# Kernel optimization log

Measured on AMD Instinct MI355X. Metric: run time of the kernel, lower is better.

## Reference

```python
import jax, jax.numpy as jnp
import numpy as np

B, S, D = 4, 2048, 2048
H = 16
Q_LORA = 1536
KV_LORA = 512
D_NOPE = 128
D_ROPE = 64
D_V = 128
MLP = 8192
EPS = 1e-6
THETA = 10000.0


def rmsnorm(x, scale, eps=EPS):
    var = jnp.mean(jnp.square(x.astype(jnp.float32)), axis=-1, keepdims=True)
    return (x * jax.lax.rsqrt(var + eps)).astype(x.dtype) * scale


def rope(x, positions):
    # x: [B, S, H, d], positions: [B, S]
    d = x.shape[-1]
    inv_freq = 1.0 / (THETA ** (jnp.arange(0, d, 2, dtype=jnp.float32) / d))
    ang = positions.astype(jnp.float32)[..., None] * inv_freq  # [B,S,d/2]
    cos = jnp.cos(ang)[:, :, None, :]
    sin = jnp.sin(ang)[:, :, None, :]
    x1, x2 = jnp.split(x, 2, axis=-1)
    return jnp.concatenate([x1 * cos - x2 * sin, x2 * cos + x1 * sin], axis=-1)


def setup_inputs() -> dict:
    key = jax.random.key(0)
    ks = jax.random.split(key, 16)
    sd = lambda fan: 1.0 / np.sqrt(fan)
    inp = {
        'inputs': jax.random.normal(ks[0], (B, S, D), jnp.float32),
        'decoder_segment_ids': jnp.ones((B, S), jnp.int32),
        'decoder_positions': jnp.broadcast_to(jnp.arange(S, dtype=jnp.int32), (B, S)),
        'pre_ln_scale': jnp.ones((D,), jnp.float32),
        'post_ln_scale': jnp.ones((D,), jnp.float32),
        'q_ln_scale': jnp.ones((Q_LORA,), jnp.float32),
        'kv_ln_scale': jnp.ones((KV_LORA,), jnp.float32),
        'wq_a': jax.random.normal(ks[1], (D, Q_LORA), jnp.float32) * sd(D),
        'wq_b': jax.random.normal(ks[2], (Q_LORA, H, D_NOPE + D_ROPE), jnp.float32) * sd(Q_LORA),
        'wkv_a': jax.random.normal(ks[3], (D, KV_LORA + D_ROPE), jnp.float32) * sd(D),
        'wkv_b': jax.random.normal(ks[4], (KV_LORA, H, D_NOPE + D_V), jnp.float32) * sd(KV_LORA),
        'wo_attn': jax.random.normal(ks[5], (H, D_V, D), jnp.float32) * sd(H * D_V),
        'wi_0': jax.random.normal(ks[6], (D, MLP), jnp.float32) * sd(D),
        'wi_1': jax.random.normal(ks[7], (D, MLP), jnp.float32) * sd(D),
        'wo_mlp': jax.random.normal(ks[8], (MLP, D), jnp.float32) * sd(MLP),
    }
    return inp


def reference(inputs, decoder_segment_ids, decoder_positions, pre_ln_scale, post_ln_scale,
              q_ln_scale, kv_ln_scale, wq_a, wq_b, wkv_a, wkv_b, wo_attn, wi_0, wi_1, wo_mlp):
    # ---- pre-norm ----
    lnx = rmsnorm(inputs, pre_ln_scale)

    # ---- MLA attention ----
    # low-rank query: down-proj, norm, up-proj
    q_c = rmsnorm(lnx @ wq_a, q_ln_scale)                       # [B,S,Q_LORA]
    q = jnp.einsum('bsr,rhd->bshd', q_c, wq_b)                  # [B,S,H,nope+rope]
    q_nope, q_rope = q[..., :D_NOPE], q[..., D_NOPE:]

    # compressed kv + decoupled rope key
    kv = lnx @ wkv_a                                            # [B,S,KV_LORA+rope]
    c_kv = rmsnorm(kv[..., :KV_LORA], kv_ln_scale)
    k_rope = kv[..., KV_LORA:][:, :, None, :]                   # [B,S,1,rope]
    kvu = jnp.einsum('bsr,rhd->bshd', c_kv, wkv_b)              # [B,S,H,nope+v]
    k_nope, v = kvu[..., :D_NOPE], kvu[..., D_NOPE:]

    q_rope = rope(q_rope, decoder_positions)
    k_rope = rope(k_rope, decoder_positions)
    k_rope = jnp.broadcast_to(k_rope, (B, S, H, D_ROPE))

    qf = jnp.concatenate([q_nope, q_rope], axis=-1)             # [B,S,H,192]
    kf = jnp.concatenate([k_nope, k_rope], axis=-1)

    scale = 1.0 / np.sqrt(D_NOPE + D_ROPE)
    scores = jnp.einsum('bqhd,bkhd->bhqk', qf, kf) * scale      # [B,H,S,S]

    pos = decoder_positions
    seg = decoder_segment_ids
    mask = (pos[:, :, None] >= pos[:, None, :]) & (seg[:, :, None] == seg[:, None, :])
    scores = jnp.where(mask[:, None, :, :], scores, -1e9)
    probs = jax.nn.softmax(scores, axis=-1)

    attn = jnp.einsum('bhqk,bkhd->bqhd', probs, v)              # [B,S,H,D_V]
    attn_out = jnp.einsum('bqhd,hdm->bqm', attn, wo_attn)       # [B,S,D]

    # ---- residual + post-norm ----
    intermediate = inputs + attn_out
    hidden = rmsnorm(intermediate, post_ln_scale)

    # ---- gated MLP (silu * linear) ----
    mlp = (jax.nn.silu(hidden @ wi_0) * (hidden @ wi_1)) @ wo_mlp

    return mlp + intermediate
```

## Files before the change

kernel.cpp:

```cpp
#include <hip/hip_runtime.h>
#include <stdint.h>

typedef unsigned short u16;
typedef __bf16 bf16x8 __attribute__((ext_vector_type(8)));
typedef float f32x4 __attribute__((ext_vector_type(4)));

#define B_ 4
#define S_ 2048
#define H_ 16
#define TOK (B_*S_)
#define MFMA_B16 __builtin_amdgcn_mfma_f32_16x16x32_bf16
#define LGKM0 asm volatile("s_waitcnt lgkmcnt(0)" ::: "memory")
#define VMC(n) asm volatile("s_waitcnt vmcnt(" #n ")" ::: "memory")

__device__ __forceinline__ u16 f32_bf16(float f) {
    union { float f; unsigned int u; } x; x.f = f;
    return (u16)((x.u + 0x7fffu + ((x.u >> 16) & 1u)) >> 16);
}
__device__ __forceinline__ float bf2f(u16 v) {
    union { unsigned int u; float f; } x; x.u = ((unsigned int)v) << 16; return x.f;
}
__device__ __forceinline__ void gld_lds16(const u16* g, u16* lds) {
    __builtin_amdgcn_global_load_lds(
        (const __attribute__((address_space(1))) unsigned int*)g,
        (__attribute__((address_space(3))) unsigned int*)lds, 16, 0, 0);
}

__global__ void fill_sentinel(float* o, int n) {
    int i = blockIdx.x * 256 + threadIdx.x;
    if (i < n) o[i] = 12345.0f;
}

__global__ __launch_bounds__(256) void transpose_f32_bf16(const float* __restrict__ in, u16* __restrict__ out,
                                                          int K, int N, int Npad) {
    __shared__ float t[32][33];
    int nb = blockIdx.x * 32, kb = blockIdx.y * 32;
    int c = threadIdx.x & 31, r = threadIdx.x >> 5;
#pragma unroll
    for (int i = 0; i < 4; ++i) {
        int kk = kb + r + i * 8, nn = nb + c;
        t[r + i * 8][c] = (kk < K && nn < N) ? in[(size_t)kk * N + nn] : 0.f;
    }
    __syncthreads();
#pragma unroll
    for (int i = 0; i < 4; ++i) {
        int no = nb + r + i * 8, ko = kb + c;
        if (no < Npad && ko < K) out[(size_t)no * K + ko] = f32_bf16(t[c][r + i * 8]);
    }
}

__global__ __launch_bounds__(256) void rmsnorm_f32(const float* __restrict__ in, const float* __restrict__ sc,
                                                   u16* __restrict__ out, int N) {
    int row = blockIdx.x;
    const float* x = in + (size_t)row * N;
    float ss = 0.f;
    for (int c = threadIdx.x * 4; c < N; c += 1024) {
        float4 v = *(const float4*)(x + c);
        ss += v.x * v.x + v.y * v.y + v.z * v.z + v.w * v.w;
    }
#pragma unroll
    for (int off = 32; off; off >>= 1) ss += __shfl_down(ss, off);
    __shared__ float red[4];
    if ((threadIdx.x & 63) == 0) red[threadIdx.x >> 6] = ss;
    __syncthreads();
    float rs = rsqrtf((red[0] + red[1] + red[2] + red[3]) / (float)N + 1e-6f);
    for (int c = threadIdx.x * 4; c < N; c += 1024) {
        float4 v = *(const float4*)(x + c);
        float4 s4 = *(const float4*)(sc + c);
        ushort4 ov;
        ov.x = f32_bf16(v.x * rs * s4.x);
        ov.y = f32_bf16(v.y * rs * s4.y);
        ov.z = f32_bf16(v.z * rs * s4.z);
        ov.w = f32_bf16(v.w * rs * s4.w);
        *(ushort4*)&out[(size_t)row * N + c] = ov;
    }
}

__global__ __launch_bounds__(256) void rmsnorm_bf16(const u16* __restrict__ in, const float* __restrict__ sc,
                                                    u16* __restrict__ out, int N) {
    int row = blockIdx.x;
    const u16* x = in + (size_t)row * N;
    float ss = 0.f;
    for (int c = threadIdx.x * 8; c < N; c += 2048) {
        ushort4 v0 = *(const ushort4*)(x + c);
        ushort4 v1 = *(const ushort4*)(x + c + 4);
        float f0 = bf2f(v0.x), f1 = bf2f(v0.y), f2 = bf2f(v0.z), f3 = bf2f(v0.w);
        float f4 = bf2f(v1.x), f5 = bf2f(v1.y), f6 = bf2f(v1.z), f7 = bf2f(v1.w);
        ss += f0*f0 + f1*f1 + f2*f2 + f3*f3 + f4*f4 + f5*f5 + f6*f6 + f7*f7;
    }
#pragma unroll
    for (int off = 32; off; off >>= 1) ss += __shfl_down(ss, off);
    __shared__ float red[4];
    if ((threadIdx.x & 63) == 0) red[threadIdx.x >> 6] = ss;
    __syncthreads();
    float rs = rsqrtf((red[0] + red[1] + red[2] + red[3]) / (float)N + 1e-6f);
    for (int c = threadIdx.x * 8; c < N; c += 2048) {
        ushort4 v0 = *(const ushort4*)(x + c);
        ushort4 v1 = *(const ushort4*)(x + c + 4);
        ushort4 o0, o1;
        o0.x = f32_bf16(bf2f(v0.x) * rs * sc[c + 0]);
        o0.y = f32_bf16(bf2f(v0.y) * rs * sc[c + 1]);
        o0.z = f32_bf16(bf2f(v0.z) * rs * sc[c + 2]);
        o0.w = f32_bf16(bf2f(v0.w) * rs * sc[c + 3]);
        o1.x = f32_bf16(bf2f(v1.x) * rs * sc[c + 4]);
        o1.y = f32_bf16(bf2f(v1.y) * rs * sc[c + 5]);
        o1.z = f32_bf16(bf2f(v1.z) * rs * sc[c + 6]);
        o1.w = f32_bf16(bf2f(v1.w) * rs * sc[c + 7]);
        *(ushort4*)&out[(size_t)row * N + c] = o0;
        *(ushort4*)&out[(size_t)row * N + c + 4] = o1;
    }
}

__global__ __launch_bounds__(128) void kv_post(const u16* __restrict__ kv, const float* __restrict__ scale,
                                               const int* __restrict__ pos, u16* __restrict__ ckv,
                                               u16* __restrict__ kr) {
    int row = blockIdx.x;
    const u16* x = kv + (size_t)row * 640;
    int c = threadIdx.x * 4;
    ushort4 v = *(const ushort4*)(x + c);
    float f0 = bf2f(v.x), f1 = bf2f(v.y), f2 = bf2f(v.z), f3 = bf2f(v.w);
    float ss = f0*f0 + f1*f1 + f2*f2 + f3*f3;
#pragma unroll
    for (int off = 32; off; off >>= 1) ss += __shfl_down(ss, off);
    __shared__ float red[2];
    if ((threadIdx.x & 63) == 0) red[threadIdx.x >> 6] = ss;
    __syncthreads();
    float rs = rsqrtf((red[0] + red[1]) * (1.f / 512.f) + 1e-6f);
    float4 s4 = *(const float4*)(scale + c);
    ushort4 ov;
    ov.x = f32_bf16(f0 * rs * s4.x);
    ov.y = f32_bf16(f1 * rs * s4.y);
    ov.z = f32_bf16(f2 * rs * s4.z);
    ov.w = f32_bf16(f3 * rs * s4.w);
    *(ushort4*)&ckv[(size_t)row * 512 + c] = ov;
    if (threadIdx.x < 32) {
        int i = threadIdx.x;
        float x1 = bf2f(x[512 + i]), x2 = bf2f(x[544 + i]);
        float inv = expf(-(float)(2 * i) * (1.f / 64.f) * 9.2103403719761836f);
        float ang = (float)pos[row] * inv;
        float sn, cs; sincosf(ang, &sn, &cs);
        kr[(size_t)row * 64 + i]      = f32_bf16(x1 * cs - x2 * sn);
        kr[(size_t)row * 64 + 32 + i] = f32_bf16(x2 * cs + x1 * sn);
    }
}

__global__ __launch_bounds__(64) void q_rope_inplace(u16* __restrict__ q, const int* __restrict__ pos) {
    int token = blockIdx.x, h = blockIdx.y;
    u16* p = q + ((size_t)token * 16 + h) * 192;
    int t = threadIdx.x, i = t & 31;
    float x1 = bf2f(p[128 + i]), x2 = bf2f(p[160 + i]);
    float inv = expf(-(float)(2 * i) * (1.f / 64.f) * 9.2103403719761836f);
    float ang = (float)pos[token] * inv;
    float sn, cs; sincosf(ang, &sn, &cs);
    float val = (t < 32) ? (x1 * cs - x2 * sn) : (x2 * cs + x1 * sn);
    p[128 + t] = f32_bf16(val);
}

__global__ __launch_bounds__(320) void kv_build(const u16* __restrict__ kvu, const u16* __restrict__ kr,
                                                u16* __restrict__ kf, u16* __restrict__ vf, int tok0) {
    int local = blockIdx.x, h = blockIdx.y;
    int token = tok0 + local;
    int b = token >> 11, s = token & 2047;
    int bh = b * 16 + h;
    int tile = s >> 6, ki = s & 63;
    const u16* u = kvu + ((size_t)local * 16 + h) * 256;
    int t = threadIdx.x;
    if (t < 192) {
        u16 val = (t < 128) ? u[t] : kr[(size_t)token * 64 + (t - 128)];
        int byte = (ki * 384 + t * 2) ^ ((ki & 7) << 4);
        kf[(size_t)bh * (S_ * 192) + (size_t)tile * 12288 + (byte >> 1)] = val;
    } else {
        int dv = t - 192;
        u16 val = u[128 + dv];
        int byte = (dv * 128 + ki * 2) ^ ((dv & 7) << 4);
        vf[(size_t)bh * (S_ * 128) + (size_t)tile * 8192 + (byte >> 1)] = val;
    }
}

__global__ __launch_bounds__(256) void gemm128(const u16* __restrict__ A, const u16* __restrict__ Bt,
                                               u16* __restrict__ C, int M, int N, int K) {
    __shared__ u16 As[128 * 32];
    __shared__ u16 Bs[128 * 32];
    const int l = threadIdx.x & 63, w = threadIdx.x >> 6;
    const int wr = w >> 1, wc = w & 1;
    const int m0 = blockIdx.y * 128, n0 = blockIdx.x * 128;
    const int lm = l & 15, lg = l >> 4;
    const int srow = l >> 2, sk = (l & 3) * 8;
    f32x4 acc[4][4] = {};
    for (int k0 = 0; k0 < K; k0 += 32) {
#pragma unroll
        for (int i = 0; i < 2; ++i) {
            int c = w * 2 + i;
            gld_lds16(A  + (size_t)(m0 + c * 16 + srow) * K + k0 + sk, &As[c * 512]);
            gld_lds16(Bt + (size_t)(n0 + c * 16 + srow) * K + k0 + sk, &Bs[c * 512]);
        }
        __syncthreads();
        bf16x8 a[4], b[4];
#pragma unroll
        for (int m = 0; m < 4; ++m) a[m] = *(const bf16x8*)&As[(wr * 64 + m * 16 + lm) * 32 + lg * 8];
#pragma unroll
        for (int n = 0; n < 4; ++n) b[n] = *(const bf16x8*)&Bs[(wc * 64 + n * 16 + lm) * 32 + lg * 8];
#pragma unroll
        for (int m = 0; m < 4; ++m)
#pragma unroll
            for (int n = 0; n < 4; ++n)
                acc[m][n] = MFMA_B16(a[m], b[n], acc[m][n], 0, 0, 0);
        __syncthreads();
    }
#pragma unroll
    for (int m = 0; m < 4; ++m)
#pragma unroll
        for (int j = 0; j < 4; ++j) {
            int row = m0 + wr * 64 + m * 16 + lg * 4 + j;
            size_t base = (size_t)row * N + n0 + wc * 64;
#pragma unroll
            for (int n = 0; n < 4; ++n)
                C[base + n * 16 + lm] = f32_bf16(acc[m][n][j]);
        }
}

template<int EPI>
__global__ __launch_bounds__(512, 1) void gemm256(const u16* __restrict__ A, const u16* __restrict__ Bt,
                                                  void* __restrict__ Cv, const void* __restrict__ Rv,
                                                  int M, int N, int K) {
    __shared__ u16 lds[65536];
    char* ldsb = (char*)lds;
    const int tid = threadIdx.x;
    const int l = tid & 63, w = tid >> 6;
    const int wr = w >> 2, wcn = w & 3;
    const int lm = l & 15, lg = l >> 4;

    const int gx = gridDim.x;
    const int nwg = gx * gridDim.y;
    const int lin = blockIdx.y * gx + blockIdx.x;
    const int swz = (lin & 7) * (nwg >> 3) + (lin >> 3);
    const int m0 = (swz / gx) * 256, n0 = (swz % gx) * 256;

    int sr[2], sc[2];
#pragma unroll
    for (int ld = 0; ld < 2; ++ld) {
        int P = tid * 16 + ld * 8192;
        sr[ld] = P >> 7;
        sc[ld] = (P & 127) ^ ((sr[ld] & 7) << 4);
    }
    const u16* Ab = A + (size_t)m0 * K;
    const u16* Bb = Bt + (size_t)n0 * K;

    f32x4 acc[8][4] = {};

    auto stage = [&](const u16* gp, int mb, int h, int t) {
#pragma unroll
        for (int ld = 0; ld < 2; ++ld)
            gld_lds16(gp + (size_t)(h * 128 + sr[ld]) * K + t * 64 + (sc[ld] >> 1),
                      (u16*)(ldsb + (t & 1) * 65536 + mb + h * 16384 + tid * 16 + ld * 8192));
    };
    auto readA = [&](int buf, int fm, int ks) -> bf16x8 {
        int m = wr * 128 + fm * 16 + lm;
        int r = m & 127;
        int byte = (ks * 64 + lg * 16) ^ ((r & 7) << 4);
        return *(const bf16x8*)(ldsb + buf * 65536 + (m >> 7) * 16384 + r * 128 + byte);
    };
    auto readB = [&](int buf, int fn, int ks) -> bf16x8 {
        int n = wcn * 64 + fn * 16 + lm;
        int r = n & 127;
        int byte = (ks * 64 + lg * 16) ^ ((r & 7) << 4);
        return *(const bf16x8*)(ldsb + buf * 65536 + 32768 + (n >> 7) * 16384 + r * 128 + byte);
    };

    const int nt = K >> 6;
    stage(Ab, 0, 0, 0); stage(Ab, 0, 1, 0);
    stage(Bb, 32768, 0, 0); stage(Bb, 32768, 1, 0);
    VMC(0);
    __builtin_amdgcn_s_barrier();

#pragma unroll 1
    for (int t = 0; t < nt; ++t) {
        const int buf = t & 1;
        const bool nx = (t + 1 < nt);
        bf16x8 a0, a1, a2, a3, a4, a5, a6, a7;
        bf16x8 b0 = readB(buf, 0, 0), b1 = readB(buf, 0, 1), b2 = readB(buf, 1, 0), b3 = readB(buf, 1, 1);
        a0 = readA(buf, 0, 0); a1 = readA(buf, 0, 1); a2 = readA(buf, 1, 0); a3 = readA(buf, 1, 1);
        a4 = readA(buf, 2, 0); a5 = readA(buf, 2, 1); a6 = readA(buf, 3, 0); a7 = readA(buf, 3, 1);
        if (nx) { stage(Ab, 0, 0, t + 1); stage(Ab, 0, 1, t + 1); }
        __builtin_amdgcn_s_barrier();
        LGKM0;
        __builtin_amdgcn_sched_barrier(0);
        __builtin_amdgcn_s_setprio(1);
        acc[0][0] = MFMA_B16(a0, b0, acc[0][0], 0, 0, 0);
        acc[0][0] = MFMA_B16(a1, b1, acc[0][0], 0, 0, 0);
        acc[0][1] = MFMA_B16(a0, b2, acc[0][1], 0, 0, 0);
        acc[0][1] = MFMA_B16(a1, b3, acc[0][1], 0, 0, 0);
        acc[1][0] = MFMA_B16(a2, b0, acc[1][0], 0, 0, 0);
        acc[1][0] = MFMA_B16(a3, b1, acc[1][0], 0, 0, 0);
        acc[1][1] = MFMA_B16(a2, b2, acc[1][1], 0, 0, 0);
        acc[1][1] = MFMA_B16(a3, b3, acc[1][1], 0, 0, 0);
        acc[2][0] = MFMA_B16(a4, b0, acc[2][0], 0, 0, 0);
        acc[2][0] = MFMA_B16(a5, b1, acc[2][0], 0, 0, 0);
        acc[2][1] = MFMA_B16(a4, b2, acc[2][1], 0, 0, 0);
        acc[2][1] = MFMA_B16(a5, b3, acc[2][1], 0, 0, 0);
        acc[3][0] = MFMA_B16(a6, b0, acc[3][0], 0, 0, 0);
        acc[3][0] = MFMA_B16(a7, b1, acc[3][0], 0, 0, 0);
        acc[3][1] = MFMA_B16(a6, b2, acc[3][1], 0, 0, 0);
        acc[3][1] = MFMA_B16(a7, b3, acc[3][1], 0, 0, 0);
        __builtin_amdgcn_s_setprio(0);
        __builtin_amdgcn_s_barrier();
        bf16x8 c0 = readB(buf, 2, 0), c1 = readB(buf, 2, 1), c2 = readB(buf, 3, 0), c3 = readB(buf, 3, 1);
        if (nx) { stage(Bb, 32768, 0, t + 1); stage(Bb, 32768, 1, t + 1); }
        __builtin_amdgcn_s_barrier();
        LGKM0;
        __builtin_amdgcn_sched_barrier(0);
        __builtin_amdgcn_s_setprio(1);
        acc[0][2] = MFMA_B16(a0, c0, acc[0][2], 0, 0, 0);
        acc[0][2] = MFMA_B16(a1, c1, acc[0][2], 0, 0, 0);
        acc[0][3] = MFMA_B16(a0, c2, acc[0][3], 0, 0, 0);
        acc[0][3] = MFMA_B16(a1, c3, acc[0][3], 0, 0, 0);
        acc[1][2] = MFMA_B16(a2, c0, acc[1][2], 0, 0, 0);
        acc[1][2] = MFMA_B16(a3, c1, acc[1][2], 0, 0, 0);
        acc[1][3] = MFMA_B16(a2, c2, acc[1][3], 0, 0, 0);
        acc[1][3] = MFMA_B16(a3, c3, acc[1][3], 0, 0, 0);
        acc[2][2] = MFMA_B16(a4, c0, acc[2][2], 0, 0, 0);
        acc[2][2] = MFMA_B16(a5, c1, acc[2][2], 0, 0, 0);
        acc[2][3] = MFMA_B16(a4, c2, acc[2][3], 0, 0, 0);
        acc[2][3] = MFMA_B16(a5, c3, acc[2][3], 0, 0, 0);
        acc[3][2] = MFMA_B16(a6, c0, acc[3][2], 0, 0, 0);
        acc[3][2] = MFMA_B16(a7, c1, acc[3][2], 0, 0, 0);
        acc[3][3] = MFMA_B16(a6, c2, acc[3][3], 0, 0, 0);
        acc[3][3] = MFMA_B16(a7, c3, acc[3][3], 0, 0, 0);
        __builtin_amdgcn_s_setprio(0);
        __builtin_amdgcn_s_barrier();
        a0 = readA(buf, 4, 0); a1 = readA(buf, 4, 1); a2 = readA(buf, 5, 0); a3 = readA(buf, 5, 1);
        a4 = readA(buf, 6, 0); a5 = readA(buf, 6, 1); a6 = readA(buf, 7, 0); a7 = readA(buf, 7, 1);
        __builtin_amdgcn_s_barrier();
        LGKM0;
        __builtin_amdgcn_sched_barrier(0);
        __builtin_amdgcn_s_setprio(1);
        acc[4][2] = MFMA_B16(a0, c0, acc[4][2], 0, 0, 0);
        acc[4][2] = MFMA_B16(a1, c1, acc[4][2], 0, 0, 0);
        acc[4][3] = MFMA_B16(a0, c2, acc[4][3], 0, 0, 0);
        acc[4][3] = MFMA_B16(a1, c3, acc[4][3], 0, 0, 0);
        acc[5][2] = MFMA_B16(a2, c0, acc[5][2], 0, 0, 0);
        acc[5][2] = MFMA_B16(a3, c1, acc[5][2], 0, 0, 0);
        acc[5][3] = MFMA_B16(a2, c2, acc[5][3], 0, 0, 0);
        acc[5][3] = MFMA_B16(a3, c3, acc[5][3], 0, 0, 0);
        acc[6][2] = MFMA_B16(a4, c0, acc[6][2], 0, 0, 0);
        acc[6][2] = MFMA_B16(a5, c1, acc[6][2], 0, 0, 0);
        acc[6][3] = MFMA_B16(a4, c2, acc[6][3], 0, 0, 0);
        acc[6][3] = MFMA_B16(a5, c3, acc[6][3], 0, 0, 0);
        acc[7][2] = MFMA_B16(a6, c0, acc[7][2], 0, 0, 0);
        acc[7][2] = MFMA_B16(a7, c1, acc[7][2], 0, 0, 0);
        acc[7][3] = MFMA_B16(a6, c2, acc[7][3], 0, 0, 0);
        acc[7][3] = MFMA_B16(a7, c3, acc[7][3], 0, 0, 0);
        __builtin_amdgcn_s_setprio(0);
        __builtin_amdgcn_s_barrier();
        VMC(0);
        __builtin_amdgcn_s_barrier();
        __builtin_amdgcn_s_setprio(1);
        acc[4][0] = MFMA_B16(a0, b0, acc[4][0], 0, 0, 0);
        acc[4][0] = MFMA_B16(a1, b1, acc[4][0], 0, 0, 0);
        acc[4][1] = MFMA_B16(a0, b2, acc[4][1], 0, 0, 0);
        acc[4][1] = MFMA_B16(a1, b3, acc[4][1], 0, 0, 0);
        acc[5][0] = MFMA_B16(a2, b0, acc[5][0], 0, 0, 0);
        acc[5][0] = MFMA_B16(a3, b1, acc[5][0], 0, 0, 0);
        acc[5][1] = MFMA_B16(a2, b2, acc[5][1], 0, 0, 0);
        acc[5][1] = MFMA_B16(a3, b3, acc[5][1], 0, 0, 0);
        acc[6][0] = MFMA_B16(a4, b0, acc[6][0], 0, 0, 0);
        acc[6][0] = MFMA_B16(a5, b1, acc[6][0], 0, 0, 0);
        acc[6][1] = MFMA_B16(a4, b2, acc[6][1], 0, 0, 0);
        acc[6][1] = MFMA_B16(a5, b3, acc[6][1], 0, 0, 0);
        acc[7][0] = MFMA_B16(a6, b0, acc[7][0], 0, 0, 0);
        acc[7][0] = MFMA_B16(a7, b1, acc[7][0], 0, 0, 0);
        acc[7][1] = MFMA_B16(a6, b2, acc[7][1], 0, 0, 0);
        acc[7][1] = MFMA_B16(a7, b3, acc[7][1], 0, 0, 0);
        __builtin_amdgcn_s_setprio(0);
        __builtin_amdgcn_s_barrier();
    }
#pragma unroll
    for (int fm = 0; fm < 8; ++fm)
#pragma unroll
        for (int j = 0; j < 4; ++j) {
            int row = m0 + wr * 128 + fm * 16 + lg * 4 + j;
            size_t base = (size_t)row * N + n0 + wcn * 64;
#pragma unroll
            for (int fn = 0; fn < 4; ++fn) {
                size_t idx = base + fn * 16 + lm;
                float v = acc[fm][fn][j];
                if (EPI == 0) {
                    ((u16*)Cv)[idx] = f32_bf16(v);
                } else if (EPI == 1) {
                    ((float*)Cv)[idx] = v + ((const float*)Rv)[idx];
                } else {
                    float x0 = bf2f(((const u16*)Rv)[idx]);
                    float sl = x0 / (1.f + expf(-x0));
                    ((u16*)Cv)[idx] = f32_bf16(sl * v);
                }
            }
        }
}

__global__ __launch_bounds__(256, 3) void attn_fwd(const u16* __restrict__ qf, const u16* __restrict__ kfs,
                                                   const u16* __restrict__ vfs, u16* __restrict__ attn) {
    __shared__ u16 Ks[64 * 192];
    __shared__ u16 Vs[128 * 64];
    __shared__ u16 Ps[4][1024];
    const int lin = blockIdx.y * gridDim.x + blockIdx.x;
    const int xcd = lin & 7, j = lin >> 3;
    const int bh = xcd * 8 + (j >> 4);
    const int px = j & 15;
    const int b = bh >> 4, h = bh & 15;
    const int l = threadIdx.x & 63, w = threadIdx.x >> 6;
    const int lm = l & 15, g = l >> 4;
    const u16* kb0 = kfs + (size_t)bh * (S_ * 192);
    const u16* vb0 = vfs + (size_t)bh * (S_ * 128);
    const float scale = 0.07216878364870322f;

    auto stageK = [&](int kt2) {
        const u16* kc = kb0 + (size_t)kt2 * 12288;
#pragma unroll
        for (int i = 0; i < 6; ++i) {
            int c = w + i * 4;
            gld_lds16(kc + c * 512 + l * 8, &Ks[c * 512]);
        }
    };
    auto stageV = [&](int kt2) {
        const u16* vc = vb0 + (size_t)kt2 * 8192;
#pragma unroll
        for (int i = 0; i < 4; ++i) {
            int c = w + i * 4;
            gld_lds16(vc + c * 512 + l * 8, &Vs[c * 512]);
        }
    };

    stageK(0);

    for (int pass = 0; pass < 2; ++pass) {
        const int qb = pass ? (31 - px) : px;
        const int qrow = qb * 64 + w * 16 + lm;
        const u16* qp = qf + (((size_t)(b * S_ + qrow)) * 16 + h) * 192 + g * 8;
        bf16x8 qr[6];
#pragma unroll
        for (int c = 0; c < 6; ++c) qr[c] = *(const bf16x8*)(qp + c * 32);
        f32x4 o[8] = {};
        float mrow[4] = {-1e30f, -1e30f, -1e30f, -1e30f};
        float lrow[4] = {0.f, 0.f, 0.f, 0.f};
        for (int kt = 0; kt <= qb; ++kt) {
            __syncthreads();
            stageV(kt);
            f32x4 sc[4] = {};
#pragma unroll
            for (int nf = 0; nf < 4; ++nf) {
                int key = nf * 16 + lm;
                int kswz = (key & 7) << 4;
#pragma unroll
                for (int c = 0; c < 6; ++c) {
                    int byte = (key * 384 + (c * 32 + g * 8) * 2) ^ kswz;
                    bf16x8 kv = *(const bf16x8*)((const char*)Ks + byte);
                    sc[nf] = MFMA_B16(qr[c], kv, sc[nf], 0, 0, 0);
                }
            }
            LGKM0;
            __builtin_amdgcn_s_barrier();
            if (kt < qb) stageK(kt + 1);
#pragma unroll
            for (int jj = 0; jj < 4; ++jj) {
                const int q_g = qb * 64 + w * 16 + g * 4 + jj;
                float mx = -1e30f;
#pragma unroll
                for (int nf = 0; nf < 4; ++nf) {
                    int key_g = kt * 64 + nf * 16 + lm;
                    float v = sc[nf][jj] * scale;
                    v = (key_g > q_g) ? -1e30f : v;
                    sc[nf][jj] = v;
                    mx = fmaxf(mx, v);
                }
                mx = fmaxf(mx, __shfl_xor(mx, 1));
                mx = fmaxf(mx, __shfl_xor(mx, 2));
                mx = fmaxf(mx, __shfl_xor(mx, 4));
                mx = fmaxf(mx, __shfl_xor(mx, 8));
                float newm = fmaxf(mrow[jj], mx);
                float fac = __expf(mrow[jj] - newm);
                mrow[jj] = newm;
                float rs = 0.f;
                u16 pb[4];
#pragma unroll
                for (int nf = 0; nf < 4; ++nf) {
                    float pv = __expf(sc[nf][jj] - newm);
                    rs += pv;
                    pb[nf] = f32_bf16(pv);
                }
                rs += __shfl_xor(rs, 1);
                rs += __shfl_xor(rs, 2);
                rs += __shfl_xor(rs, 4);
                rs += __shfl_xor(rs, 8);
                lrow[jj] = lrow[jj] * fac + rs;
#pragma unroll
                for (int n = 0; n < 8; ++n) o[n][jj] *= fac;
                int row = g * 4 + jj;
                int rswz = (row & 7) << 4;
#pragma unroll
                for (int nf = 0; nf < 4; ++nf) {
                    int byte = (row * 128 + (nf * 16 + lm) * 2) ^ rswz;
                    *(u16*)((char*)&Ps[w][0] + byte) = pb[nf];
                }
            }
            if (kt < qb) { VMC(6); } else { VMC(0); }
            __builtin_amdgcn_s_barrier();
            __builtin_amdgcn_sched_barrier(0);
#pragma unroll
            for (int kc2 = 0; kc2 < 2; ++kc2) {
                int pbyte = (lm * 128 + (kc2 * 32 + g * 8) * 2) ^ ((lm & 7) << 4);
                bf16x8 pa = *(const bf16x8*)((const char*)&Ps[w][0] + pbyte);
#pragma unroll
                for (int n = 0; n < 8; ++n) {
                    int dv = n * 16 + lm;
                    int vbyte = (dv * 128 + (kc2 * 32 + g * 8) * 2) ^ ((dv & 7) << 4);
                    bf16x8 vv = *(const bf16x8*)((const char*)Vs + vbyte);
                    o[n] = MFMA_B16(pa, vv, o[n], 0, 0, 0);
                }
            }
        }
#pragma unroll
        for (int jj = 0; jj < 4; ++jj) {
            float inv = 1.f / lrow[jj];
            int s = qb * 64 + w * 16 + g * 4 + jj;
            size_t base = ((size_t)(b * S_ + s)) * (H_ * 128) + h * 128;
#pragma unroll
            for (int n = 0; n < 8; ++n)
                attn[base + n * 16 + lm] = f32_bf16(o[n][jj] * inv);
        }
        if (pass == 0) stageK(0);
    }
}

extern "C" void kernel_launch(void* const* d_in, const int* in_sizes, int n_in,
                              void* d_out, int out_size, void* d_ws, size_t ws_size,
                              hipStream_t stream) {
    (void)in_sizes; (void)n_in;
    const float* inputs = (const float*)d_in[0];
    const int*   pos    = (const int*)d_in[2];
    const float* pre_s  = (const float*)d_in[3];
    const float* post_s = (const float*)d_in[4];
    const float* q_s    = (const float*)d_in[5];
    const float* kv_s   = (const float*)d_in[6];
    const float* wq_a   = (const float*)d_in[7];
    const float* wq_b   = (const float*)d_in[8];
    const float* wkv_a  = (const float*)d_in[9];
    const float* wkv_b  = (const float*)d_in[10];
    const float* wo_at  = (const float*)d_in[11];
    const float* wi0    = (const float*)d_in[12];
    const float* wi1    = (const float*)d_in[13];
    const float* wom    = (const float*)d_in[14];
    float* out = (float*)d_out;

    char* p = (char*)d_ws;
    auto alloc = [&](size_t n) { char* r = p; p += (n + 255) & ~(size_t)255; return r; };
    char* R1   = alloc((size_t)134217728);
    u16* vf    = (u16*)alloc((size_t)33554432);
    u16* aslot = (u16*)alloc((size_t)33554432);
    u16* wslot = (u16*)alloc((size_t)33554432);
    u16* ckv   = (u16*)alloc((size_t)8388608);
    u16* krope = (u16*)alloc((size_t)1048576);
    if ((size_t)(p - (char*)d_ws) > ws_size) {
        fill_sentinel<<<(out_size + 255) / 256, 256, 0, stream>>>(out, out_size);
        return;
    }
    u16* kf    = (u16*)R1;
    u16* q_c   = (u16*)R1;
    u16* kvtmp = (u16*)(R1 + 25165824);
    u16* q     = (u16*)(R1 + 50331648);
    u16* lnx   = (u16*)(R1 + 100663296);
    u16* kvu   = (u16*)(R1 + 100663296);
    u16* X     = (u16*)R1;

    rmsnorm_f32<<<TOK, 256, 0, stream>>>(inputs, pre_s, lnx, 2048);
    transpose_f32_bf16<<<dim3(48, 64), 256, 0, stream>>>(wq_a, wslot, 2048, 1536, 1536);
    gemm256<0><<<dim3(6, 32), 512, 0, stream>>>(lnx, wslot, q_c, nullptr, TOK, 1536, 2048);
    rmsnorm_bf16<<<TOK, 256, 0, stream>>>(q_c, q_s, q_c, 1536);
    transpose_f32_bf16<<<dim3(20, 64), 256, 0, stream>>>(wkv_a, wslot, 2048, 576, 640);
    gemm128<<<dim3(5, 64), 256, 0, stream>>>(lnx, wslot, kvtmp, TOK, 640, 2048);
    kv_post<<<TOK, 128, 0, stream>>>(kvtmp, kv_s, pos, ckv, krope);
    transpose_f32_bf16<<<dim3(96, 48), 256, 0, stream>>>(wq_b, wslot, 1536, 3072, 3072);
    gemm256<0><<<dim3(12, 32), 512, 0, stream>>>(q_c, wslot, q, nullptr, TOK, 3072, 1536);
    q_rope_inplace<<<dim3(TOK, 16), 64, 0, stream>>>(q, pos);
    transpose_f32_bf16<<<dim3(128, 16), 256, 0, stream>>>(wkv_b, wslot, 512, 4096, 4096);
    for (int ch = 0; ch < 2; ++ch) {
        int t0 = ch * 4096;
        gemm256<0><<<dim3(16, 16), 512, 0, stream>>>(ckv + (size_t)t0 * 512, wslot, kvu, nullptr, 4096, 4096, 512);
        kv_build<<<dim3(4096, 16), 320, 0, stream>>>(kvu, krope, kf, vf, t0);
    }
    attn_fwd<<<dim3(16, 64), 256, 0, stream>>>(q, kf, vf, aslot);
    transpose_f32_bf16<<<dim3(64, 64), 256, 0, stream>>>(wo_at, wslot, 2048, 2048, 2048);
    gemm256<1><<<dim3(8, 32), 512, 0, stream>>>(aslot, wslot, out, inputs, TOK, 2048, 2048);
    rmsnorm_f32<<<TOK, 256, 0, stream>>>(out, post_s, aslot, 2048);
    transpose_f32_bf16<<<dim3(256, 64), 256, 0, stream>>>(wi0, wslot, 2048, 8192, 8192);
    gemm256<0><<<dim3(32, 32), 512, 0, stream>>>(aslot, wslot, X, nullptr, TOK, 8192, 2048);
    transpose_f32_bf16<<<dim3(256, 64), 256, 0, stream>>>(wi1, wslot, 2048, 8192, 8192);
    gemm256<2><<<dim3(32, 32), 512, 0, stream>>>(aslot, wslot, X, X, TOK, 8192, 2048);
    transpose_f32_bf16<<<dim3(64, 256), 256, 0, stream>>>(wom, wslot, 8192, 2048, 2048);
    gemm256<1><<<dim3(8, 32), 512, 0, stream>>>(X, wslot, out, out, TOK, 2048, 8192);
}
```

Baseline: 1.666 ms.

## Restage GEMM LDS tiles into four quarter units with finer-grained vmcnt waits

The 256x256 GEMM's shared-memory staging is split into four 16KB units, each matched to the sub-tile a particular MFMA phase consumes. Each unit's next-tile prefetch is issued in a different phase, and partial vmcnt waits let compute start before all loads have landed, instead of one full wait per iteration. The swizzled workgroup-to-tile mapping is removed in favour of plain blockIdx mapping, which may change L2 reuse across workgroups. The new ordering assumes in-order vmcnt completion per unit, so the counts must exactly match the issue order.

```diff
diff --git a/kernel.cpp b/kernel.cpp
--- a/kernel.cpp
+++ b/kernel.cpp
@@ -12,6 +12,7 @@
 #define MFMA_B16 __builtin_amdgcn_mfma_f32_16x16x32_bf16
 #define LGKM0 asm volatile("s_waitcnt lgkmcnt(0)" ::: "memory")
 #define VMC(n) asm volatile("s_waitcnt vmcnt(" #n ")" ::: "memory")
+#define SB0 __builtin_amdgcn_sched_barrier(0)
 
 __device__ __forceinline__ u16 f32_bf16(float f) {
     union { float f; unsigned int u; } x; x.f = f;
@@ -229,48 +230,46 @@
     const int l = tid & 63, w = tid >> 6;
     const int wr = w >> 2, wcn = w & 3;
     const int lm = l & 15, lg = l >> 4;
-
-    const int gx = gridDim.x;
-    const int nwg = gx * gridDim.y;
-    const int lin = blockIdx.y * gx + blockIdx.x;
-    const int swz = (lin & 7) * (nwg >> 3) + (lin >> 3);
-    const int m0 = (swz / gx) * 256, n0 = (swz % gx) * 256;
-
-    int sr[2], sc[2];
+    const int m0 = blockIdx.y * 256, n0 = blockIdx.x * 256;
+
+    int sr[2], scb[2];
 #pragma unroll
     for (int ld = 0; ld < 2; ++ld) {
         int P = tid * 16 + ld * 8192;
         sr[ld] = P >> 7;
-        sc[ld] = (P & 127) ^ ((sr[ld] & 7) << 4);
+        scb[ld] = (P & 127) ^ ((sr[ld] & 7) << 4);
     }
     const u16* Ab = A + (size_t)m0 * K;
     const u16* Bb = Bt + (size_t)n0 * K;
 
     f32x4 acc[8][4] = {};
 
-    auto stage = [&](const u16* gp, int mb, int h, int t) {
-#pragma unroll
-        for (int ld = 0; ld < 2; ++ld)
-            gld_lds16(gp + (size_t)(h * 128 + sr[ld]) * K + t * 64 + (sc[ld] >> 1),
-                      (u16*)(ldsb + (t & 1) * 65536 + mb + h * 16384 + tid * 16 + ld * 8192));
+    auto stageU = [&](int unit, int tt) {
+#pragma unroll
+        for (int ld = 0; ld < 2; ++ld) {
+            int r = sr[ld];
+            const u16* src;
+            if (unit == 0)      src = Ab + (size_t)((r >> 6) * 128 + (r & 63)) * K + tt * 64 + (scb[ld] >> 1);
+            else if (unit == 1) src = Ab + (size_t)((r >> 6) * 128 + 64 + (r & 63)) * K + tt * 64 + (scb[ld] >> 1);
+            else if (unit == 2) src = Bb + (size_t)((r >> 5) * 64 + (r & 31)) * K + tt * 64 + (scb[ld] >> 1);
+            else                src = Bb + (size_t)((r >> 5) * 64 + 32 + (r & 31)) * K + tt * 64 + (scb[ld] >> 1);
+            gld_lds16(src, (u16*)(ldsb + (tt & 1) * 65536 + unit * 16384 + tid * 16 + ld * 8192));
+        }
     };
     auto readA = [&](int buf, int fm, int ks) -> bf16x8 {
-        int m = wr * 128 + fm * 16 + lm;
-        int r = m & 127;
-        int byte = (ks * 64 + lg * 16) ^ ((r & 7) << 4);
-        return *(const bf16x8*)(ldsb + buf * 65536 + (m >> 7) * 16384 + r * 128 + byte);
+        int lr = wr * 64 + (fm & 3) * 16 + lm;
+        int byte = lr * 128 + ((ks * 64 + lg * 16) ^ ((lr & 7) << 4));
+        return *(const bf16x8*)(ldsb + buf * 65536 + (fm >> 2) * 16384 + byte);
     };
     auto readB = [&](int buf, int fn, int ks) -> bf16x8 {
-        int n = wcn * 64 + fn * 16 + lm;
-        int r = n & 127;
-        int byte = (ks * 64 + lg * 16) ^ ((r & 7) << 4);
-        return *(const bf16x8*)(ldsb + buf * 65536 + 32768 + (n >> 7) * 16384 + r * 128 + byte);
+        int lr = wcn * 32 + (fn & 1) * 16 + lm;
+        int byte = lr * 128 + ((ks * 64 + lg * 16) ^ ((lr & 7) << 4));
+        return *(const bf16x8*)(ldsb + buf * 65536 + (2 + (fn >> 1)) * 16384 + byte);
     };
 
     const int nt = K >> 6;
-    stage(Ab, 0, 0, 0); stage(Ab, 0, 1, 0);
-    stage(Bb, 32768, 0, 0); stage(Bb, 32768, 1, 0);
-    VMC(0);
+    stageU(0, 0); stageU(2, 0); stageU(3, 0); stageU(1, 0);
+    VMC(2);
     __builtin_amdgcn_s_barrier();
 
 #pragma unroll 1
@@ -281,10 +280,10 @@
         bf16x8 b0 = readB(buf, 0, 0), b1 = readB(buf, 0, 1), b2 = readB(buf, 1, 0), b3 = readB(buf, 1, 1);
         a0 = readA(buf, 0, 0); a1 = readA(buf, 0, 1); a2 = readA(buf, 1, 0); a3 = readA(buf, 1, 1);
         a4 = readA(buf, 2, 0); a5 = readA(buf, 2, 1); a6 = readA(buf, 3, 0); a7 = readA(buf, 3, 1);
-        if (nx) { stage(Ab, 0, 0, t + 1); stage(Ab, 0, 1, t + 1); }
+        if (nx) stageU(0, t + 1);
         __builtin_amdgcn_s_barrier();
         LGKM0;
-        __builtin_amdgcn_sched_barrier(0);
+        SB0;
         __builtin_amdgcn_s_setprio(1);
         acc[0][0] = MFMA_B16(a0, b0, acc[0][0], 0, 0, 0);
         acc[0][0] = MFMA_B16(a1, b1, acc[0][0], 0, 0, 0);
@@ -305,10 +304,10 @@
         __builtin_amdgcn_s_setprio(0);
         __builtin_amdgcn_s_barrier();
         bf16x8 c0 = readB(buf, 2, 0), c1 = readB(buf, 2, 1), c2 = readB(buf, 3, 0), c3 = readB(buf, 3, 1);
-        if (nx) { stage(Bb, 32768, 0, t + 1); stage(Bb, 32768, 1, t + 1); }
+        if (nx) { stageU(2, t + 1); VMC(4); } else { VMC(0); }
         __builtin_amdgcn_s_barrier();
         LGKM0;
-        __builtin_amdgcn_sched_barrier(0);
+        SB0;
         __builtin_amdgcn_s_setprio(1);
         acc[0][2] = MFMA_B16(a0, c0, acc[0][2], 0, 0, 0);
         acc[0][2] = MFMA_B16(a1, c1, acc[0][2], 0, 0, 0);
@@ -330,9 +329,10 @@
         __builtin_amdgcn_s_barrier();
         a0 = readA(buf, 4, 0); a1 = readA(buf, 4, 1); a2 = readA(buf, 5, 0); a3 = readA(buf, 5, 1);
         a4 = readA(buf, 6, 0); a5 = readA(buf, 6, 1); a6 = readA(buf, 7, 0); a7 = readA(buf, 7, 1);
+        if (nx) stageU(3, t + 1);
         __builtin_amdgcn_s_barrier();
         LGKM0;
-        __builtin_amdgcn_sched_barrier(0);
+        SB0;
         __builtin_amdgcn_s_setprio(1);
         acc[4][2] = MFMA_B16(a0, c0, acc[4][2], 0, 0, 0);
         acc[4][2] = MFMA_B16(a1, c1, acc[4][2], 0, 0, 0);
@@ -352,8 +352,9 @@
         acc[7][3] = MFMA_B16(a7, c3, acc[7][3], 0, 0, 0);
         __builtin_amdgcn_s_setprio(0);
         __builtin_amdgcn_s_barrier();
-        VMC(0);
-        __builtin_amdgcn_s_barrier();
+        if (nx) { stageU(1, t + 1); VMC(2); }
+        __builtin_amdgcn_s_barrier();
+        SB0;
         __builtin_amdgcn_s_setprio(1);
         acc[4][0] = MFMA_B16(a0, b0, acc[4][0], 0, 0, 0);
         acc[4][0] = MFMA_B16(a1, b1, acc[4][0], 0, 0, 0);
@@ -504,7 +505,7 @@
             }
             if (kt < qb) { VMC(6); } else { VMC(0); }
             __builtin_amdgcn_s_barrier();
-            __builtin_amdgcn_sched_barrier(0);
+            SB0;
 #pragma unroll
             for (int kc2 = 0; kc2 < 2; ++kc2) {
                 int pbyte = (lm * 128 + (kc2 * 32 + g * 8) * 2) ^ ((lm & 7) << 4);
```

Result: no change. 1.669 ms (+0.2%).
